# Optimization experiments

Measured on AMD Instinct MI355X. Metric: run time of the kernel, lower is better.

## Reference

```python
import jax, jax.numpy as jnp
import numpy as np

B = 32768
SF = 40  # subframe_size


def _gru_cell(x, h, wih, whh):
    # PyTorch GRUCell (bias=False): gates ordered [r; z; n]
    gi = x @ wih.T
    gh = h @ whh.T
    ir, iz, inn = jnp.split(gi, 3, axis=-1)
    hr, hz, hn = jnp.split(gh, 3, axis=-1)
    r = jax.nn.sigmoid(ir + hr)
    z = jax.nn.sigmoid(iz + hz)
    n = jnp.tanh(inn + r * hn)
    return (1.0 - z) * n + z * h


def setup_inputs() -> dict:
    key = jax.random.key(0)
    ks = iter(jax.random.split(key, 32))

    def rn(shape, scale=None):
        s = scale if scale is not None else 1.0 / np.sqrt(shape[-1])
        return (jax.random.normal(next(ks), shape, dtype=jnp.float32) * s)

    inp = {
        'cond': rn((B, 80), 1.0),
        'prev_pred': rn((B, 256), 1.0),
        'exc_mem': rn((B, 256), 1.0),
        'period': 32.0 + 223.0 * jax.random.uniform(next(ks), (B,), dtype=jnp.float32),
        's1': rn((B, 160), 1.0),
        's2': rn((B, 128), 1.0),
        's3': rn((B, 128), 1.0),
        's4': rn((B, 164), 1.0),
        'w_gain': rn((1, 80)),
        'b_gain': jnp.zeros((1,), jnp.float32),
        'w_fwc0': rn((192, 328)),
        'w_fwc0_glu': rn((192, 192)),
        'wih1': rn((480, 272)),
        'whh1': rn((480, 160)),
        'wglu1': rn((160, 160)),
        'wih2': rn((384, 240)),
        'whh2': rn((384, 128)),
        'wglu2': rn((128, 128)),
        'wih3': rn((384, 208)),
        'whh3': rn((384, 128)),
        'wglu3': rn((128, 128)),
        'w_skip': rn((128, 688)),
        'w_skip_glu': rn((128, 128)),
        'w_sig': rn((40, 128)),
        'w_pg': rn((4, 192)),
        'b_pg': jnp.zeros((4,), jnp.float32),
    }
    return inp


def reference(cond, prev_pred, exc_mem, period, s1, s2, s3, s4,
              w_gain, b_gain, w_fwc0, w_fwc0_glu,
              wih1, whh1, wglu1, wih2, whh2, wglu2, wih3, whh3, wglu3,
              w_skip, w_skip_glu, w_sig, w_pg, b_pg):
    # eval mode (training=False): quantization noise is identity; compat_mode=False path
    dt = cond.dtype
    period = jnp.clip(jnp.nan_to_num(period, nan=128.0, posinf=128.0, neginf=128.0), 32.0, 255.0)
    rng = jnp.arange(SF + 4, dtype=dt)
    # fractional pitch lookup with linear interpolation into exc_mem
    idxf = 256.0 - period[:, None] + rng[None, :] - 2.0  # [B, SF+4]
    idx0 = jnp.floor(idxf)
    alpha = jnp.clip(idxf - idx0, 0.0, 1.0)
    W = exc_mem.shape[1]
    i0 = jnp.mod(jnp.clip(idx0, 0.0, 255.0).astype(jnp.int32), W)
    i1 = jnp.mod(jnp.clip(idx0 + 1.0, 0.0, 255.0).astype(jnp.int32), W)
    v0 = jnp.take_along_axis(exc_mem, i0, axis=1)
    v1 = jnp.take_along_axis(exc_mem, i1, axis=1)
    pred = (1.0 - alpha) * v0 + alpha * v1  # [B, SF+4]

    # bounded gain
    gain = 0.2 + 0.8 * jax.nn.sigmoid(cond @ w_gain.T + b_gain)
    gain = jnp.clip(jnp.nan_to_num(gain, nan=1.0, posinf=20.0, neginf=1e-3), 1e-3, 20.0)
    inv = 1.0 / (1e-5 + gain)
    pred_n = pred * inv
    prev = exc_mem[:, -SF:] * inv
    tmp = jnp.concatenate([cond, pred_n, prev], axis=1)  # [B, 164]
    fpitch = pred_n[:, 2:-2]  # [B, SF]

    # FWConv: linear over cat(state, x), tanh, GLU
    xcat = jnp.concatenate([s4, tmp], axis=1)  # [B, 328]
    fw = jnp.tanh(xcat @ w_fwc0.T)
    fwc0_out = fw * jax.nn.sigmoid(fw @ w_fwc0_glu.T)  # [B, 192]
    new_s4 = tmp

    pitch_gain = jax.nn.sigmoid(fwc0_out @ w_pg.T + b_pg)  # [B, 4]

    h1 = _gru_cell(jnp.concatenate([fwc0_out, pitch_gain[:, 0:1] * fpitch, prev], 1), s1, wih1, whh1)
    g1 = h1 * jax.nn.sigmoid(h1 @ wglu1.T)
    h2 = _gru_cell(jnp.concatenate([g1, pitch_gain[:, 1:2] * fpitch, prev], 1), s2, wih2, whh2)
    g2 = h2 * jax.nn.sigmoid(h2 @ wglu2.T)
    h3 = _gru_cell(jnp.concatenate([g2, pitch_gain[:, 2:3] * fpitch, prev], 1), s3, wih3, whh3)
    g3 = h3 * jax.nn.sigmoid(h3 @ wglu3.T)

    skip_in = jnp.concatenate([g1, g2, g3, fwc0_out, pitch_gain[:, 3:4] * fpitch, prev], 1)  # [B, 688]
    sk = jnp.tanh(skip_in @ w_skip.T)
    sk = sk * jax.nn.sigmoid(sk @ w_skip_glu.T)
    sig_out = jnp.tanh(sk @ w_sig.T) * gain  # [B, SF]

    exc_mem_new = jnp.concatenate([exc_mem[:, SF:], sig_out], 1)
    prev_pred_new = jnp.concatenate([prev_pred[:, SF:], pred[:, 2:2 + SF]], 1)
    return sig_out, exc_mem_new, prev_pred_new, h1, h2, h3, new_s4
```

## Files before the change

kernel.cpp:

```cpp
#include <hip/hip_runtime.h>
#include <cstdint>
#include <cmath>

#define BTOT 32768L
#define OSIG 0L
#define OEXC (BTOT*40L)
#define OPREV (OEXC + BTOT*256L)
#define OH1 (OPREV + BTOT*256L)
#define OH2 (OH1 + BTOT*160L)
#define OH3 (OH2 + BTOT*128L)
#define ONS4 (OH3 + BTOT*128L)

typedef __attribute__((ext_vector_type(8))) short short8;
typedef __attribute__((ext_vector_type(4))) short short4v;
typedef __attribute__((ext_vector_type(4))) float f32x4;

#define AP 968


#define W_F0     0L
#define W_F0G    67584L
#define W_PG     104448L
#define W_IH1R   107520L
#define W_IH1Z   162816L
#define W_IH1N   218112L
#define W_HH1R   273408L
#define W_HH1Z   310272L
#define W_HH1N   347136L
#define W_GLU1   384000L
#define W_IH2R   420864L
#define W_IH2Z   453632L
#define W_IH2N   486400L
#define W_HH2R   519168L
#define W_HH2Z   535552L
#define W_HH2N   551936L
#define W_GLU2   568320L
#define W_IH3R   584704L
#define W_IH3Z   613376L
#define W_IH3N   642048L
#define W_HH3R   670720L
#define W_HH3Z   687104L
#define W_HH3N   703488L
#define W_GLU3   719872L
#define W_SKIP   736256L
#define W_SKIPG  859136L
#define W_SIG    875520L

__device__ __forceinline__ float sigm(float x){ return 1.0f/(1.0f+__expf(-x)); }
__device__ __forceinline__ float tanh_f(float x){
    float e = __expf(2.0f*x);
    return 1.0f - 2.0f/(e+1.0f);
}
__device__ __forceinline__ uint16_t f2bf(float x){
    union { float f; uint32_t u; } v; v.f = x;
    uint32_t r = v.u + 0x7FFFu + ((v.u>>16)&1u);
    return (uint16_t)(r>>16);
}
__device__ __forceinline__ float bf2f(uint16_t h){
    union { float f; uint32_t u; } v; v.u = ((uint32_t)h)<<16;
    return v.f;
}
__device__ __forceinline__ short4v pack4(float4 v){
    short4v r;
    r.x=(short)f2bf(v.x); r.y=(short)f2bf(v.y); r.z=(short)f2bf(v.z); r.w=(short)f2bf(v.w);
    return r;
}

struct PrepArgs { const float* s[15]; };

__global__ __launch_bounds__(64) void prep_kernel(PrepArgs pa, uint16_t* dst){
    static const long J[27][8] = {
        {0,  0,192,328,352,192, W_F0,   0},
        {1,  0,192,192,192,192, W_F0G,  0},
        {13, 0,  4,192,192, 16, W_PG,   0},
        {2,  0,160,272,288,192, W_IH1R, 0},
        {2,160,160,272,288,192, W_IH1Z, 0},
        {2,320,160,272,288,192, W_IH1N, 0},
        {3,  0,160,160,192,192, W_HH1R, 0},
        {3,160,160,160,192,192, W_HH1Z, 0},
        {3,320,160,160,192,192, W_HH1N, 0},
        {4,  0,160,160,192,192, W_GLU1, 0},
        {5,  0,128,240,256,128, W_IH2R, 0},
        {5,128,128,240,256,128, W_IH2Z, 0},
        {5,256,128,240,256,128, W_IH2N, 0},
        {6,  0,128,128,128,128, W_HH2R, 0},
        {6,128,128,128,128,128, W_HH2Z, 0},
        {6,256,128,128,128,128, W_HH2N, 0},
        {7,  0,128,128,128,128, W_GLU2, 0},
        {8,  0,128,208,224,128, W_IH3R, 0},
        {8,128,128,208,224,128, W_IH3Z, 0},
        {8,256,128,208,224,128, W_IH3N, 0},
        {9,  0,128,128,128,128, W_HH3R, 0},
        {9,128,128,128,128,128, W_HH3Z, 0},
        {9,256,128,128,128,128, W_HH3N, 0},
        {10, 0,128,128,128,128, W_GLU3, 0},
        {11, 0,128,688,960,128, W_SKIP, 1},
        {12, 0,128,128,128,128, W_SKIPG,0},
        {14, 0, 40,128,128, 64, W_SIG,  0},
    };
    long row = blockIdx.x;
    int j = 0;
    while (row >= J[j][5]) { row -= J[j][5]; ++j; }
    const float* src = pa.s[J[j][0]];
    const long ro = J[j][1], N = J[j][2], K = J[j][3], KP = J[j][4];
    const int type = (int)J[j][7];
    uint16_t* d = dst + J[j][6] + row*KP;
    for (long k = threadIdx.x; k < KP; k += 64){
        float v = 0.0f;
        if (row < N){
            if (type == 0){
                if (k < K) v = src[(ro+row)*K + k];
            } else {
                long s = -1;
                if (k < 192) s = 416 + k;
                else if (k >= 232 && k < 272) s = 648 + (k-232);
                else if (k >= 288 && k < 448) s = (k-288);
                else if (k >= 544 && k < 672) s = 160 + (k-544);
                else if (k >= 768 && k < 896) s = 288 + (k-768);
                else if (k >= 896 && k < 936) s = 608 + (k-896);
                if (s >= 0) v = src[row*688 + s];
            }
        }
        d[k] = f2bf(v);
    }
}

template<int KS, int CNT>
__device__ __forceinline__ void wgemm4(f32x4 (&acc)[CNT][4],
    const uint16_t* __restrict__ Bw, int KP,
    const uint16_t* A, int P, int w, int r16, int g)
{
    constexpr int T = KS*CNT;
    constexpr int PF = (T < 6) ? T : 6;
    const uint16_t* ap = A + r16*P + g*8;
    const uint16_t* bbase = Bw + (size_t)(w*16 + r16)*KP + g*8;
    short8 ring[PF];
    #pragma unroll
    for (int t=0;t<PF;++t)
        ring[t] = *(const short8*)(bbase + (size_t)(t%CNT)*128*KP + (size_t)(t/CNT)*32);
    short8 af[4];
    #pragma unroll
    for (int t=0;t<T;++t){
        const int s = t/CNT, i = t%CNT;
        if (i==0){
            #pragma unroll
            for (int mt=0;mt<4;++mt) af[mt] = *(const short8*)(ap + mt*16*P + s*32);
        }
        short8 bf = ring[t%PF];
        if (t+PF < T)
            ring[t%PF] = *(const short8*)(bbase + (size_t)((t+PF)%CNT)*128*KP + (size_t)((t+PF)/CNT)*32);
        #pragma unroll
        for (int mt=0;mt<4;++mt)
            acc[i][mt] = __builtin_amdgcn_mfma_f32_16x16x32_bf16(af[mt], bf, acc[i][mt],0,0,0);
    }
}
template<int CNT> __device__ __forceinline__ void zacc(f32x4 (&a)[CNT][4]){
    f32x4 z4 = {0.f,0.f,0.f,0.f};
    #pragma unroll
    for (int i=0;i<CNT;++i){
        #pragma unroll
        for (int mt=0;mt<4;++mt) a[i][mt]=z4;
    }
}

template<int CNT>
__device__ __forceinline__ void gru1_h(const uint16_t* __restrict__ W, uint16_t* ACTp,
    const float* __restrict__ s1g, float* __restrict__ out,
    float (&hk)[2][4][4], int row0, int w, int r16, int g)
{
    f32x4 gx[CNT][4], gh[CNT][4], ra[CNT][4], za[CNT][4];
    zacc(gx); zacc(gh); zacc(ra); zacc(za);
    wgemm4<9,CNT>(gx, W+W_IH1N, 288, ACTp,     AP, w,r16,g);
    wgemm4<9,CNT>(ra, W+W_IH1R, 288, ACTp,     AP, w,r16,g);
    wgemm4<9,CNT>(za, W+W_IH1Z, 288, ACTp,     AP, w,r16,g);
    wgemm4<6,CNT>(gh, W+W_HH1N, 192, ACTp+544, AP, w,r16,g);
    wgemm4<6,CNT>(ra, W+W_HH1R, 192, ACTp+544, AP, w,r16,g);
    wgemm4<6,CNT>(za, W+W_HH1Z, 192, ACTp+544, AP, w,r16,g);
    #pragma unroll
    for (int i=0;i<CNT;++i){
        int n = (w+8*i)*16 + r16;
        #pragma unroll
        for (int mt=0;mt<4;++mt){
            #pragma unroll
            for (int q=0;q<4;++q){
                int mrow = mt*16+g*4+q;
                float h = 0.f;
                if (n < 160){
                    float hpv = s1g[(long)(row0+mrow)*160 + n];
                    float r = sigm(ra[i][mt][q]);
                    float z = sigm(za[i][mt][q]);
                    float nn = tanh_f(gx[i][mt][q] + r*gh[i][mt][q]);
                    h = (1.f-z)*nn + z*hpv;
                    out[OH1 + (long)(row0+mrow)*160 + n] = h;
                }
                hk[i][mt][q] = h;
                ACTp[mrow*AP+768+n] = f2bf(h);
            }
        }
    }
}
template<int CNT>
__device__ __forceinline__ void glu1(const uint16_t* __restrict__ W, uint16_t* ACTp,
                                     float (&hk)[2][4][4], int w, int r16, int g){
    f32x4 gl[CNT][4];
    zacc(gl);
    wgemm4<6,CNT>(gl, W+W_GLU1, 192, ACTp+768, AP, w,r16,g);
    #pragma unroll
    for (int i=0;i<CNT;++i){
        int n = (w+8*i)*16 + r16;
        if (n < 160){
            #pragma unroll
            for (int mt=0;mt<4;++mt)
                #pragma unroll
                for (int q=0;q<4;++q){
                    int mrow = mt*16+g*4+q;
                    ACTp[mrow*AP + 288 + n] = f2bf(hk[i][mt][q]*sigm(gl[i][mt][q]));
                }
        }
    }
}

template<int KSX, int KSH>
__device__ __forceinline__ void gru23_h(
    const uint16_t* __restrict__ Wxr, const uint16_t* __restrict__ Wxz, const uint16_t* __restrict__ Wxn, int KPX,
    const uint16_t* __restrict__ Whr, const uint16_t* __restrict__ Whz, const uint16_t* __restrict__ Whn, int KPH,
    const uint16_t* XA, const uint16_t* HA, int HAP,
    const float* __restrict__ sg, float* __restrict__ outp, long obase,
    uint16_t* HBdst, int HBpitch,
    float (&hk)[4][4], int row0, int w, int r16, int g)
{
    const int n = w*16 + r16;
    f32x4 gx[1][4], gh[1][4], ra[1][4], za[1][4];
    zacc(gx); zacc(gh); zacc(ra); zacc(za);
    wgemm4<KSX,1>(gx, Wxn, KPX, XA, AP, w,r16,g);
    wgemm4<KSX,1>(ra, Wxr, KPX, XA, AP, w,r16,g);
    wgemm4<KSX,1>(za, Wxz, KPX, XA, AP, w,r16,g);
    wgemm4<KSH,1>(gh, Whn, KPH, HA, HAP, w,r16,g);
    wgemm4<KSH,1>(ra, Whr, KPH, HA, HAP, w,r16,g);
    wgemm4<KSH,1>(za, Whz, KPH, HA, HAP, w,r16,g);
    #pragma unroll
    for (int mt=0;mt<4;++mt){
        #pragma unroll
        for (int q=0;q<4;++q){
            int mrow = mt*16+g*4+q;
            float hpv = sg[(long)(row0+mrow)*128 + n];
            float r = sigm(ra[0][mt][q]), z = sigm(za[0][mt][q]);
            float nn = tanh_f(gx[0][mt][q] + r*gh[0][mt][q]);
            float h = (1.f-z)*nn + z*hpv;
            outp[obase + (long)(row0+mrow)*128 + n] = h;
            hk[mt][q] = h;
            if (HBdst) HBdst[mrow*HBpitch + n] = f2bf(h);
        }
    }
}

extern "C" __global__ __launch_bounds__(512, 2)
void fargan_mfma(const float* __restrict__ cond, const float* __restrict__ prev_pred,
                 const float* __restrict__ exc_mem, const float* __restrict__ period,
                 const float* __restrict__ s1, const float* __restrict__ s2,
                 const float* __restrict__ s3, const float* __restrict__ s4,
                 const float* __restrict__ w_gain, const float* __restrict__ b_gain,
                 const float* __restrict__ b_pg,
                 const uint16_t* __restrict__ W, float* __restrict__ out)
{
    __shared__ __align__(16) uint16_t ACT[64*AP];
    __shared__ __align__(16) uint16_t SH[64*136];
    __shared__ uint16_t FPITCHb[64*40];
    __shared__ float GAIN[64];
    __shared__ float PGs[64][4];

    const int tid = threadIdx.x;
    const int row0 = blockIdx.x * 64;
    const int w = tid >> 6, l = tid & 63, r16 = l & 15, g = l >> 4;
    const int rr = tid >> 3, c8 = tid & 7;
    const long grow = row0 + rr;

    const float* exc_row = exc_mem + grow*256;

    float a0 = 0.f;
    {
        const float4* c4 = (const float4*)(cond + grow*80);
        const float4* g4 = (const float4*)w_gain;
        float4* on4 = (float4*)(out + ONS4 + grow*164);
        for (int i=c8;i<20;i+=8){
            float4 cv = c4[i], gv = g4[i];
            a0 += cv.x*gv.x + cv.y*gv.y + cv.z*gv.z + cv.w*gv.w;
            *(short4v*)&ACT[rr*AP + 164 + 4*i] = pack4(cv);
            on4[i] = cv;
        }
    }
    a0 += __shfl_xor(a0,4,8); a0 += __shfl_xor(a0,2,8); a0 += __shfl_xor(a0,1,8);
    float gn = 0.2f + 0.8f*sigm(a0 + b_gain[0]);
    if (!(gn==gn)) gn = 1.0f;
    gn = fminf(fmaxf(gn, 0.001f), 20.0f);
    float inv = 1.0f/(1e-5f+gn);
    if (c8==0) GAIN[rr] = gn;

    float p = period[grow];
    p = (fabsf(p) <= 3.0e38f) ? p : 128.0f;
    p = fminf(fmaxf(p, 32.0f), 255.0f);

    for (int e=c8;e<44;e+=8){
        float idxf = 254.0f - p + (float)e;
        float idx0 = floorf(idxf);
        float al = fminf(fmaxf(idxf-idx0, 0.f), 1.f);
        int i0 = (int)fminf(fmaxf(idx0, 0.f), 255.f);
        int i1 = (int)fminf(fmaxf(idx0+1.f, 0.f), 255.f);
        float pr = (1.f-al)*exc_row[i0] + al*exc_row[i1];
        float pn = pr*inv;
        ACT[rr*AP + 244 + e] = f2bf(pn);
        out[ONS4 + grow*164 + 80 + e] = pn;
        if (e>=2 && e<42){
            out[OPREV + grow*256 + 216 + (e-2)] = pr;
            FPITCHb[rr*40 + (e-2)] = f2bf(pn);
        }
    }
    {
        const float4* pv4 = (const float4*)(exc_row + 216);
        float4* onp = (float4*)(out + ONS4 + grow*164 + 124);
        for (int i=c8;i<10;i+=8){
            float4 v = pv4[i];
            v.x*=inv; v.y*=inv; v.z*=inv; v.w*=inv;
            *(short4v*)&ACT[rr*AP + 288 + 4*i] = pack4(v);
            onp[i] = v;
        }
    }
    {
        const float4* s44 = (const float4*)(s4 + grow*164);
        for (int i=c8;i<41;i+=8)
            *(short4v*)&ACT[rr*AP + 4*i] = pack4(s44[i]);
        const float4* s14 = (const float4*)(s1 + grow*160);
        for (int i=c8;i<40;i+=8)
            *(short4v*)&ACT[rr*AP + 544 + 4*i] = pack4(s14[i]);
    }
    for (int i=328+c8;i<352;i+=8) ACT[rr*AP + i] = 0;
    for (int i=704+c8;i<736;i+=8) ACT[rr*AP + i] = 0;
    {
        const float4* pp4 = (const float4*)(prev_pred + grow*256 + 40);
        const float4* ex4 = (const float4*)(exc_row + 40);
        float4* op4 = (float4*)(out + OPREV + grow*256);
        float4* oe4 = (float4*)(out + OEXC + grow*256);
        for (int i=c8;i<54;i+=8){ op4[i] = pp4[i]; oe4[i] = ex4[i]; }
    }
    __syncthreads();

    float fwk[2][4][4];

    if (w < 4){
        f32x4 av[2][4]; zacc(av);
        wgemm4<11,2>(av, W+W_F0, 352, ACT, AP, w,r16,g);
        #pragma unroll
        for (int i=0;i<2;++i){
            int n = (w+8*i)*16 + r16;
            #pragma unroll
            for (int mt=0;mt<4;++mt)
                #pragma unroll
                for (int q=0;q<4;++q){
                    int mrow = mt*16+g*4+q;
                    float t = tanh_f(av[i][mt][q]);
                    fwk[i][mt][q] = t;
                    ACT[mrow*AP+352+n] = f2bf(t);
                }
        }
    } else {
        f32x4 av[1][4]; zacc(av);
        wgemm4<11,1>(av, W+W_F0, 352, ACT, AP, w,r16,g);
        int n = w*16 + r16;
        #pragma unroll
        for (int mt=0;mt<4;++mt)
            #pragma unroll
            for (int q=0;q<4;++q){
                int mrow = mt*16+g*4+q;
                float t = tanh_f(av[0][mt][q]);
                fwk[0][mt][q] = t;
                ACT[mrow*AP+352+n] = f2bf(t);
            }
    }
    __syncthreads();

    if (w < 4){
        f32x4 av[2][4]; zacc(av);
        wgemm4<6,2>(av, W+W_F0G, 192, ACT+352, AP, w,r16,g);
        #pragma unroll
        for (int i=0;i<2;++i){
            int n = (w+8*i)*16 + r16;
            #pragma unroll
            for (int mt=0;mt<4;++mt)
                #pragma unroll
                for (int q=0;q<4;++q){
                    int mrow = mt*16+g*4+q;
                    ACT[mrow*AP+n] = f2bf(fwk[i][mt][q]*sigm(av[i][mt][q]));
                }
        }
    } else {
        f32x4 av[1][4]; zacc(av);
        wgemm4<6,1>(av, W+W_F0G, 192, ACT+352, AP, w,r16,g);
        int n = w*16 + r16;
        #pragma unroll
        for (int mt=0;mt<4;++mt)
            #pragma unroll
            for (int q=0;q<4;++q){
                int mrow = mt*16+g*4+q;
                ACT[mrow*AP+n] = f2bf(fwk[0][mt][q]*sigm(av[0][mt][q]));
            }
    }
    __syncthreads();

    {
        f32x4 av[1][4]; zacc(av);
        wgemm4<6,1>(av, W+W_PG, 192, ACT, AP, 0, r16, g);
        if (w==0 && r16<4){
            float bp = b_pg[r16];
            #pragma unroll
            for (int mt=0;mt<4;++mt)
                #pragma unroll
                for (int q=0;q<4;++q)
                    PGs[mt*16+g*4+q][r16] = sigm(av[0][mt][q] + bp);
        }
    }
    __syncthreads();

    for (int i=c8;i<40;i+=8){
        ACT[rr*AP+192+i] = f2bf(PGs[rr][0]*bf2f(FPITCHb[rr*40+i]));
        ACT[rr*AP+232+i] = ACT[rr*AP+288+i];
    }
    __syncthreads();

    float hk1[2][4][4];
    if (w < 4) gru1_h<2>(W, ACT, s1, out, hk1, row0, w,r16,g);
    else       gru1_h<1>(W, ACT, s1, out, hk1, row0, w,r16,g);
    __syncthreads();

    if (w < 4) glu1<2>(W, ACT, hk1, w,r16,g); else glu1<1>(W, ACT, hk1, w,r16,g);
    {
        const float4* s24 = (const float4*)(s2 + grow*128);
        for (int i=c8;i<32;i+=8)
            *(short4v*)&ACT[rr*AP + 544 + 4*i] = pack4(s24[i]);
    }
    for (int i=c8;i<40;i+=8){
        ACT[rr*AP+448+i] = f2bf(PGs[rr][1]*bf2f(FPITCHb[rr*40+i]));
        ACT[rr*AP+488+i] = ACT[rr*AP+232+i];
    }
    for (int i=528+c8;i<544;i+=8) ACT[rr*AP+i] = 0;
    __syncthreads();

    float hk[4][4];
    gru23_h<8,4>(W+W_IH2R, W+W_IH2Z, W+W_IH2N, 256,
                 W+W_HH2R, W+W_HH2Z, W+W_HH2N, 128,
                 ACT+288, ACT+544, AP, s2, out, OH2,
                 ACT+768, AP, hk, row0, w,r16,g);
    __syncthreads();

    {
        f32x4 gl[1][4]; zacc(gl);
        wgemm4<4,1>(gl, W+W_GLU2, 128, ACT+768, AP, w,r16,g);
        int n = w*16 + r16;
        #pragma unroll
        for (int mt=0;mt<4;++mt)
            #pragma unroll
            for (int q=0;q<4;++q){
                int mrow = mt*16+g*4+q;
                ACT[mrow*AP+544+n] = f2bf(hk[mt][q]*sigm(gl[0][mt][q]));
            }
    }
    {
        const float4* s34 = (const float4*)(s3 + grow*128);
        for (int i=c8;i<32;i+=8)
            *(short4v*)&SH[rr*136 + 4*i] = pack4(s34[i]);
    }
    for (int i=c8;i<40;i+=8){
        ACT[rr*AP+672+i] = f2bf(PGs[rr][2]*bf2f(FPITCHb[rr*40+i]));
        ACT[rr*AP+712+i] = ACT[rr*AP+232+i];
    }
    for (int i=752+c8;i<768;i+=8) ACT[rr*AP+i] = 0;
    __syncthreads();

    gru23_h<7,4>(W+W_IH3R, W+W_IH3Z, W+W_IH3N, 224,
                 W+W_HH3R, W+W_HH3Z, W+W_HH3N, 128,
                 ACT+544, SH, 136, s3, out, OH3,
                 (uint16_t*)nullptr, 0, hk, row0, w,r16,g);
    __syncthreads();

    {
        int n = w*16 + r16;
        #pragma unroll
        for (int mt=0;mt<4;++mt)
            #pragma unroll
            for (int q=0;q<4;++q)
                SH[(mt*16+g*4+q)*136 + n] = f2bf(hk[mt][q]);
    }
    __syncthreads();

    {
        f32x4 gl[1][4]; zacc(gl);
        {
            const uint16_t* ap = SH + r16*136 + g*8;
            const uint16_t* bbase = W + W_GLU3 + (size_t)(w*16 + r16)*128 + g*8;
            short8 ring[4];
            #pragma unroll
            for (int t=0;t<4;++t) ring[t] = *(const short8*)(bbase + t*32);
            #pragma unroll
            for (int s=0;s<4;++s){
                short8 af[4];
                #pragma unroll
                for (int mt=0;mt<4;++mt) af[mt] = *(const short8*)(ap + mt*16*136 + s*32);
                short8 bf = ring[s];
                #pragma unroll
                for (int mt=0;mt<4;++mt)
                    gl[0][mt] = __builtin_amdgcn_mfma_f32_16x16x32_bf16(af[mt], bf, gl[0][mt],0,0,0);
            }
        }
        int n = w*16 + r16;
        #pragma unroll
        for (int mt=0;mt<4;++mt)
            #pragma unroll
            for (int q=0;q<4;++q){
                int mrow = mt*16+g*4+q;
                ACT[mrow*AP+768+n] = f2bf(hk[mt][q]*sigm(gl[0][mt][q]));
            }
    }
    for (int i=c8;i<40;i+=8)
        ACT[rr*AP+896+i] = f2bf(PGs[rr][3]*bf2f(FPITCHb[rr*40+i]));
    __syncthreads();

    float skk[4][4];
    {
        f32x4 av[1][4]; zacc(av);
        wgemm4<30,1>(av, W+W_SKIP, 960, ACT, AP, w,r16,g);
        int n = w*16 + r16;
        #pragma unroll
        for (int mt=0;mt<4;++mt)
            #pragma unroll
            for (int q=0;q<4;++q){
                int mrow = mt*16+g*4+q;
                float t = tanh_f(av[0][mt][q]);
                skk[mt][q] = t;
                SH[mrow*136+n] = f2bf(t);
            }
    }
    __syncthreads();
    {
        f32x4 av[1][4]; zacc(av);
        {
            const uint16_t* ap = SH + r16*136 + g*8;
            const uint16_t* bbase = W + W_SKIPG + (size_t)(w*16 + r16)*128 + g*8;
            short8 ring[4];
            #pragma unroll
            for (int t=0;t<4;++t) ring[t] = *(const short8*)(bbase + t*32);
            #pragma unroll
            for (int s=0;s<4;++s){
                short8 af[4];
                #pragma unroll
                for (int mt=0;mt<4;++mt) af[mt] = *(const short8*)(ap + mt*16*136 + s*32);
                short8 bf = ring[s];
                #pragma unroll
                for (int mt=0;mt<4;++mt)
                    av[0][mt] = __builtin_amdgcn_mfma_f32_16x16x32_bf16(af[mt], bf, av[0][mt],0,0,0);
            }
        }
        int n = w*16 + r16;
        #pragma unroll
        for (int mt=0;mt<4;++mt)
            #pragma unroll
            for (int q=0;q<4;++q){
                int mrow = mt*16+g*4+q;
                ACT[mrow*AP+n] = f2bf(skk[mt][q]*sigm(av[0][mt][q]));
            }
    }
    __syncthreads();
    if (w < 4){
        f32x4 av[1][4]; zacc(av);
        wgemm4<4,1>(av, W+W_SIG, 128, ACT, AP, w,r16,g);
        int n = w*16 + r16;
        if (n < 40){
            #pragma unroll
            for (int mt=0;mt<4;++mt)
                #pragma unroll
                for (int q=0;q<4;++q){
                    int mrow = mt*16+g*4+q;
                    float sv = tanh_f(av[0][mt][q]) * GAIN[mrow];
                    out[OSIG + (long)(row0+mrow)*40 + n] = sv;
                    out[OEXC + (long)(row0+mrow)*256 + 216 + n] = sv;
                }
        }
    }
}

extern "C" void kernel_launch(void* const* d_in, const int* in_sizes, int n_in,
                              void* d_out, int out_size, void* d_ws, size_t ws_size,
                              hipStream_t stream) {
    const float* cond      = (const float*)d_in[0];
    const float* prev_pred = (const float*)d_in[1];
    const float* exc_mem   = (const float*)d_in[2];
    const float* period    = (const float*)d_in[3];
    const float* s1        = (const float*)d_in[4];
    const float* s2        = (const float*)d_in[5];
    const float* s3        = (const float*)d_in[6];
    const float* s4        = (const float*)d_in[7];
    const float* w_gain    = (const float*)d_in[8];
    const float* b_gain    = (const float*)d_in[9];
    const float* w_fwc0    = (const float*)d_in[10];
    const float* w_fwc0_glu= (const float*)d_in[11];
    const float* wih1      = (const float*)d_in[12];
    const float* whh1      = (const float*)d_in[13];
    const float* wglu1     = (const float*)d_in[14];
    const float* wih2      = (const float*)d_in[15];
    const float* whh2      = (const float*)d_in[16];
    const float* wglu2     = (const float*)d_in[17];
    const float* wih3      = (const float*)d_in[18];
    const float* whh3      = (const float*)d_in[19];
    const float* wglu3     = (const float*)d_in[20];
    const float* w_skip    = (const float*)d_in[21];
    const float* w_skip_glu= (const float*)d_in[22];
    const float* w_sig     = (const float*)d_in[23];
    const float* w_pg      = (const float*)d_in[24];
    const float* b_pg      = (const float*)d_in[25];
    float* out = (float*)d_out;
    uint16_t* wsbf = (uint16_t*)d_ws;

    PrepArgs pa;
    pa.s[0]=w_fwc0; pa.s[1]=w_fwc0_glu; pa.s[2]=wih1; pa.s[3]=whh1; pa.s[4]=wglu1;
    pa.s[5]=wih2; pa.s[6]=whh2; pa.s[7]=wglu2; pa.s[8]=wih3; pa.s[9]=whh3;
    pa.s[10]=wglu3; pa.s[11]=w_skip; pa.s[12]=w_skip_glu; pa.s[13]=w_pg; pa.s[14]=w_sig;

    hipLaunchKernelGGL(prep_kernel, dim3(3856), dim3(64), 0, stream, pa, wsbf);
    hipLaunchKernelGGL(fargan_mfma, dim3(512), dim3(512), 0, stream,
        cond, prev_pred, exc_mem, period, s1, s2, s3, s4,
        w_gain, b_gain, b_pg, wsbf, out);
}
```

Baseline: 227.7 us.

## Halve per-block batch rows to 32 and double grid for occupancy

Shrinks each workgroup's batch tile from 64 to 32 rows, halving the MFMA accumulator tiles per wave and shared-memory footprint, doubles the grid to 1024 blocks, and raises launch bounds to allow 4 blocks per CU. Thread-to-row mapping for the elementwise staging loops changes from 8 to 16 threads per row. It also swaps the manual bf16 rounding for the HIP intrinsic. Each weight fragment now feeds half as many MFMAs, so weight load traffic per row doubles; the goal is more parallelism across the 256 CUs and better latency hiding.

```diff
diff --git a/kernel.cpp b/kernel.cpp
--- a/kernel.cpp
+++ b/kernel.cpp
@@ -1,4 +1,5 @@
 #include <hip/hip_runtime.h>
+#include <hip/hip_bf16.h>
 #include <cstdint>
 #include <cmath>
 
@@ -16,7 +17,6 @@
 typedef __attribute__((ext_vector_type(4))) float f32x4;
 
 #define AP 968
-
 
 #define W_F0     0L
 #define W_F0G    67584L
@@ -52,9 +52,8 @@
     return 1.0f - 2.0f/(e+1.0f);
 }
 __device__ __forceinline__ uint16_t f2bf(float x){
-    union { float f; uint32_t u; } v; v.f = x;
-    uint32_t r = v.u + 0x7FFFu + ((v.u>>16)&1u);
-    return (uint16_t)(r>>16);
+    __hip_bfloat16 h = __float2bfloat16(x);
+    return *(uint16_t*)&h;
 }
 __device__ __forceinline__ float bf2f(uint16_t h){
     union { float f; uint32_t u; } v; v.u = ((uint32_t)h)<<16;
@@ -126,7 +125,7 @@
 }
 
 template<int KS, int CNT>
-__device__ __forceinline__ void wgemm4(f32x4 (&acc)[CNT][4],
+__device__ __forceinline__ void wgemm4(f32x4 (&acc)[CNT][2],
     const uint16_t* __restrict__ Bw, int KP,
     const uint16_t* A, int P, int w, int r16, int g)
 {
@@ -138,37 +137,37 @@
     #pragma unroll
     for (int t=0;t<PF;++t)
         ring[t] = *(const short8*)(bbase + (size_t)(t%CNT)*128*KP + (size_t)(t/CNT)*32);
-    short8 af[4];
+    short8 af[2];
     #pragma unroll
     for (int t=0;t<T;++t){
         const int s = t/CNT, i = t%CNT;
         if (i==0){
             #pragma unroll
-            for (int mt=0;mt<4;++mt) af[mt] = *(const short8*)(ap + mt*16*P + s*32);
+            for (int mt=0;mt<2;++mt) af[mt] = *(const short8*)(ap + mt*16*P + s*32);
         }
         short8 bf = ring[t%PF];
         if (t+PF < T)
             ring[t%PF] = *(const short8*)(bbase + (size_t)((t+PF)%CNT)*128*KP + (size_t)((t+PF)/CNT)*32);
         #pragma unroll
-        for (int mt=0;mt<4;++mt)
+        for (int mt=0;mt<2;++mt)
             acc[i][mt] = __builtin_amdgcn_mfma_f32_16x16x32_bf16(af[mt], bf, acc[i][mt],0,0,0);
     }
 }
-template<int CNT> __device__ __forceinline__ void zacc(f32x4 (&a)[CNT][4]){
+template<int CNT> __device__ __forceinline__ void zacc(f32x4 (&a)[CNT][2]){
     f32x4 z4 = {0.f,0.f,0.f,0.f};
     #pragma unroll
     for (int i=0;i<CNT;++i){
         #pragma unroll
-        for (int mt=0;mt<4;++mt) a[i][mt]=z4;
+        for (int mt=0;mt<2;++mt) a[i][mt]=z4;
     }
 }
 
 template<int CNT>
 __device__ __forceinline__ void gru1_h(const uint16_t* __restrict__ W, uint16_t* ACTp,
     const float* __restrict__ s1g, float* __restrict__ out,
-    float (&hk)[2][4][4], int row0, int w, int r16, int g)
+    float (&hk)[2][2][4], int row0, int w, int r16, int g)
 {
-    f32x4 gx[CNT][4], gh[CNT][4], ra[CNT][4], za[CNT][4];
+    f32x4 gx[CNT][2], gh[CNT][2], ra[CNT][2], za[CNT][2];
     zacc(gx); zacc(gh); zacc(ra); zacc(za);
     wgemm4<9,CNT>(gx, W+W_IH1N, 288, ACTp,     AP, w,r16,g);
     wgemm4<9,CNT>(ra, W+W_IH1R, 288, ACTp,     AP, w,r16,g);
@@ -180,7 +179,7 @@
     for (int i=0;i<CNT;++i){
         int n = (w+8*i)*16 + r16;
         #pragma unroll
-        for (int mt=0;mt<4;++mt){
+        for (int mt=0;mt<2;++mt){
             #pragma unroll
             for (int q=0;q<4;++q){
                 int mrow = mt*16+g*4+q;
@@ -201,8 +200,8 @@
 }
 template<int CNT>
 __device__ __forceinline__ void glu1(const uint16_t* __restrict__ W, uint16_t* ACTp,
-                                     float (&hk)[2][4][4], int w, int r16, int g){
-    f32x4 gl[CNT][4];
+                                     float (&hk)[2][2][4], int w, int r16, int g){
+    f32x4 gl[CNT][2];
     zacc(gl);
     wgemm4<6,CNT>(gl, W+W_GLU1, 192, ACTp+768, AP, w,r16,g);
     #pragma unroll
@@ -210,7 +209,7 @@
         int n = (w+8*i)*16 + r16;
         if (n < 160){
             #pragma unroll
-            for (int mt=0;mt<4;++mt)
+            for (int mt=0;mt<2;++mt)
                 #pragma unroll
                 for (int q=0;q<4;++q){
                     int mrow = mt*16+g*4+q;
@@ -227,10 +226,10 @@
     const uint16_t* XA, const uint16_t* HA, int HAP,
     const float* __restrict__ sg, float* __restrict__ outp, long obase,
     uint16_t* HBdst, int HBpitch,
-    float (&hk)[4][4], int row0, int w, int r16, int g)
+    float (&hk)[2][4], int row0, int w, int r16, int g)
 {
     const int n = w*16 + r16;
-    f32x4 gx[1][4], gh[1][4], ra[1][4], za[1][4];
+    f32x4 gx[1][2], gh[1][2], ra[1][2], za[1][2];
     zacc(gx); zacc(gh); zacc(ra); zacc(za);
     wgemm4<KSX,1>(gx, Wxn, KPX, XA, AP, w,r16,g);
     wgemm4<KSX,1>(ra, Wxr, KPX, XA, AP, w,r16,g);
@@ -239,7 +238,7 @@
     wgemm4<KSH,1>(ra, Whr, KPH, HA, HAP, w,r16,g);
     wgemm4<KSH,1>(za, Whz, KPH, HA, HAP, w,r16,g);
     #pragma unroll
-    for (int mt=0;mt<4;++mt){
+    for (int mt=0;mt<2;++mt){
         #pragma unroll
         for (int q=0;q<4;++q){
             int mrow = mt*16+g*4+q;
@@ -254,7 +253,7 @@
     }
 }
 
-extern "C" __global__ __launch_bounds__(512, 2)
+extern "C" __global__ __launch_bounds__(512, 4)
 void fargan_mfma(const float* __restrict__ cond, const float* __restrict__ prev_pred,
                  const float* __restrict__ exc_mem, const float* __restrict__ period,
                  const float* __restrict__ s1, const float* __restrict__ s2,
@@ -263,16 +262,16 @@
                  const float* __restrict__ b_pg,
                  const uint16_t* __restrict__ W, float* __restrict__ out)
 {
-    __shared__ __align__(16) uint16_t ACT[64*AP];
-    __shared__ __align__(16) uint16_t SH[64*136];
-    __shared__ uint16_t FPITCHb[64*40];
-    __shared__ float GAIN[64];
-    __shared__ float PGs[64][4];
+    __shared__ __align__(16) uint16_t ACT[32*AP];
+    __shared__ __align__(16) uint16_t SH[32*136];
+    __shared__ uint16_t FPITCHb[32*40];
+    __shared__ float GAIN[32];
+    __shared__ float PGs[32][4];
 
     const int tid = threadIdx.x;
-    const int row0 = blockIdx.x * 64;
+    const int row0 = blockIdx.x * 32;
     const int w = tid >> 6, l = tid & 63, r16 = l & 15, g = l >> 4;
-    const int rr = tid >> 3, c8 = tid & 7;
+    const int rr = tid >> 4, c16 = tid & 15;
     const long grow = row0 + rr;
 
     const float* exc_row = exc_mem + grow*256;
@@ -282,25 +281,26 @@
         const float4* c4 = (const float4*)(cond + grow*80);
         const float4* g4 = (const float4*)w_gain;
         float4* on4 = (float4*)(out + ONS4 + grow*164);
-        for (int i=c8;i<20;i+=8){
+        for (int i=c16;i<20;i+=16){
             float4 cv = c4[i], gv = g4[i];
             a0 += cv.x*gv.x + cv.y*gv.y + cv.z*gv.z + cv.w*gv.w;
             *(short4v*)&ACT[rr*AP + 164 + 4*i] = pack4(cv);
             on4[i] = cv;
         }
     }
-    a0 += __shfl_xor(a0,4,8); a0 += __shfl_xor(a0,2,8); a0 += __shfl_xor(a0,1,8);
+    a0 += __shfl_xor(a0,8,16); a0 += __shfl_xor(a0,4,16);
+    a0 += __shfl_xor(a0,2,16); a0 += __shfl_xor(a0,1,16);
     float gn = 0.2f + 0.8f*sigm(a0 + b_gain[0]);
     if (!(gn==gn)) gn = 1.0f;
     gn = fminf(fmaxf(gn, 0.001f), 20.0f);
     float inv = 1.0f/(1e-5f+gn);
-    if (c8==0) GAIN[rr] = gn;
+    if (c16==0) GAIN[rr] = gn;
 
     float p = period[grow];
     p = (fabsf(p) <= 3.0e38f) ? p : 128.0f;
     p = fminf(fmaxf(p, 32.0f), 255.0f);
 
-    for (int e=c8;e<44;e+=8){
+    for (int e=c16;e<44;e+=16){
         float idxf = 254.0f - p + (float)e;
         float idx0 = floorf(idxf);
         float al = fminf(fmaxf(idxf-idx0, 0.f), 1.f);
@@ -318,7 +318,7 @@
     {
         const float4* pv4 = (const float4*)(exc_row + 216);
         float4* onp = (float4*)(out + ONS4 + grow*164 + 124);
-        for (int i=c8;i<10;i+=8){
+        for (int i=c16;i<10;i+=16){
             float4 v = pv4[i];
             v.x*=inv; v.y*=inv; v.z*=inv; v.w*=inv;
             *(short4v*)&ACT[rr*AP + 288 + 4*i] = pack4(v);
@@ -327,33 +327,33 @@
     }
     {
         const float4* s44 = (const float4*)(s4 + grow*164);
-        for (int i=c8;i<41;i+=8)
+        for (int i=c16;i<41;i+=16)
             *(short4v*)&ACT[rr*AP + 4*i] = pack4(s44[i]);
         const float4* s14 = (const float4*)(s1 + grow*160);
-        for (int i=c8;i<40;i+=8)
+        for (int i=c16;i<40;i+=16)
             *(short4v*)&ACT[rr*AP + 544 + 4*i] = pack4(s14[i]);
     }
-    for (int i=328+c8;i<352;i+=8) ACT[rr*AP + i] = 0;
-    for (int i=704+c8;i<736;i+=8) ACT[rr*AP + i] = 0;
+    for (int i=328+c16;i<352;i+=16) ACT[rr*AP + i] = 0;
+    for (int i=704+c16;i<736;i+=16) ACT[rr*AP + i] = 0;
     {
         const float4* pp4 = (const float4*)(prev_pred + grow*256 + 40);
         const float4* ex4 = (const float4*)(exc_row + 40);
         float4* op4 = (float4*)(out + OPREV + grow*256);
         float4* oe4 = (float4*)(out + OEXC + grow*256);
-        for (int i=c8;i<54;i+=8){ op4[i] = pp4[i]; oe4[i] = ex4[i]; }
-    }
-    __syncthreads();
-
-    float fwk[2][4][4];
+        for (int i=c16;i<54;i+=16){ op4[i] = pp4[i]; oe4[i] = ex4[i]; }
+    }
+    __syncthreads();
+
+    float fwk[2][2][4];
 
     if (w < 4){
-        f32x4 av[2][4]; zacc(av);
+        f32x4 av[2][2]; zacc(av);
         wgemm4<11,2>(av, W+W_F0, 352, ACT, AP, w,r16,g);
         #pragma unroll
         for (int i=0;i<2;++i){
             int n = (w+8*i)*16 + r16;
             #pragma unroll
-            for (int mt=0;mt<4;++mt)
+            for (int mt=0;mt<2;++mt)
                 #pragma unroll
                 for (int q=0;q<4;++q){
                     int mrow = mt*16+g*4+q;
@@ -363,11 +363,11 @@
                 }
         }
     } else {
-        f32x4 av[1][4]; zacc(av);
+        f32x4 av[1][2]; zacc(av);
         wgemm4<11,1>(av, W+W_F0, 352, ACT, AP, w,r16,g);
         int n = w*16 + r16;
         #pragma unroll
-        for (int mt=0;mt<4;++mt)
+        for (int mt=0;mt<2;++mt)
             #pragma unroll
             for (int q=0;q<4;++q){
                 int mrow = mt*16+g*4+q;
@@ -379,13 +379,13 @@
     __syncthreads();
 
     if (w < 4){
-        f32x4 av[2][4]; zacc(av);
+        f32x4 av[2][2]; zacc(av);
         wgemm4<6,2>(av, W+W_F0G, 192, ACT+352, AP, w,r16,g);
         #pragma unroll
         for (int i=0;i<2;++i){
             int n = (w+8*i)*16 + r16;
             #pragma unroll
-            for (int mt=0;mt<4;++mt)
+            for (int mt=0;mt<2;++mt)
                 #pragma unroll
                 for (int q=0;q<4;++q){
                     int mrow = mt*16+g*4+q;
@@ -393,11 +393,11 @@
                 }
         }
     } else {
-        f32x4 av[1][4]; zacc(av);
+        f32x4 av[1][2]; zacc(av);
         wgemm4<6,1>(av, W+W_F0G, 192, ACT+352, AP, w,r16,g);
         int n = w*16 + r16;
         #pragma unroll
-        for (int mt=0;mt<4;++mt)
+        for (int mt=0;mt<2;++mt)
             #pragma unroll
             for (int q=0;q<4;++q){
                 int mrow = mt*16+g*4+q;
@@ -407,12 +407,12 @@
     __syncthreads();
 
     {
-        f32x4 av[1][4]; zacc(av);
+        f32x4 av[1][2]; zacc(av);
         wgemm4<6,1>(av, W+W_PG, 192, ACT, AP, 0, r16, g);
         if (w==0 && r16<4){
             float bp = b_pg[r16];
             #pragma unroll
-            for (int mt=0;mt<4;++mt)
+            for (int mt=0;mt<2;++mt)
                 #pragma unroll
                 for (int q=0;q<4;++q)
                     PGs[mt*16+g*4+q][r16] = sigm(av[0][mt][q] + bp);
@@ -420,13 +420,13 @@
     }
     __syncthreads();
 
-    for (int i=c8;i<40;i+=8){
+    for (int i=c16;i<40;i+=16){
         ACT[rr*AP+192+i] = f2bf(PGs[rr][0]*bf2f(FPITCHb[rr*40+i]));
         ACT[rr*AP+232+i] = ACT[rr*AP+288+i];
     }
     __syncthreads();
 
-    float hk1[2][4][4];
+    float hk1[2][2][4];
     if (w < 4) gru1_h<2>(W, ACT, s1, out, hk1, row0, w,r16,g);
     else       gru1_h<1>(W, ACT, s1, out, hk1, row0, w,r16,g);
     __syncthreads();
@@ -434,17 +434,17 @@
     if (w < 4) glu1<2>(W, ACT, hk1, w,r16,g); else glu1<1>(W, ACT, hk1, w,r16,g);
     {
         const float4* s24 = (const float4*)(s2 + grow*128);
-        for (int i=c8;i<32;i+=8)
+        for (int i=c16;i<32;i+=16)
             *(short4v*)&ACT[rr*AP + 544 + 4*i] = pack4(s24[i]);
     }
-    for (int i=c8;i<40;i+=8){
+    for (int i=c16;i<40;i+=16){
         ACT[rr*AP+448+i] = f2bf(PGs[rr][1]*bf2f(FPITCHb[rr*40+i]));
         ACT[rr*AP+488+i] = ACT[rr*AP+232+i];
     }
-    for (int i=528+c8;i<544;i+=8) ACT[rr*AP+i] = 0;
-    __syncthreads();
-
-    float hk[4][4];
+    for (int i=528+c16;i<544;i+=16) ACT[rr*AP+i] = 0;
+    __syncthreads();
+
+    float hk[2][4];
     gru23_h<8,4>(W+W_IH2R, W+W_IH2Z, W+W_IH2N, 256,
                  W+W_HH2R, W+W_HH2Z, W+W_HH2N, 128,
                  ACT+288, ACT+544, AP, s2, out, OH2,
@@ -452,11 +452,11 @@
     __syncthreads();
 
     {
-        f32x4 gl[1][4]; zacc(gl);
+        f32x4 gl[1][2]; zacc(gl);
         wgemm4<4,1>(gl, W+W_GLU2, 128, ACT+768, AP, w,r16,g);
         int n = w*16 + r16;
         #pragma unroll
-        for (int mt=0;mt<4;++mt)
+        for (int mt=0;mt<2;++mt)
             #pragma unroll
             for (int q=0;q<4;++q){
                 int mrow = mt*16+g*4+q;
@@ -465,14 +465,14 @@
     }
     {
         const float4* s34 = (const float4*)(s3 + grow*128);
-        for (int i=c8;i<32;i+=8)
+        for (int i=c16;i<32;i+=16)
             *(short4v*)&SH[rr*136 + 4*i] = pack4(s34[i]);
     }
-    for (int i=c8;i<40;i+=8){
+    for (int i=c16;i<40;i+=16){
         ACT[rr*AP+672+i] = f2bf(PGs[rr][2]*bf2f(FPITCHb[rr*40+i]));
         ACT[rr*AP+712+i] = ACT[rr*AP+232+i];
     }
-    for (int i=752+c8;i<768;i+=8) ACT[rr*AP+i] = 0;
+    for (int i=752+c16;i<768;i+=16) ACT[rr*AP+i] = 0;
     __syncthreads();
 
     gru23_h<7,4>(W+W_IH3R, W+W_IH3Z, W+W_IH3N, 224,
@@ -484,7 +484,7 @@
     {
         int n = w*16 + r16;
         #pragma unroll
-        for (int mt=0;mt<4;++mt)
+        for (int mt=0;mt<2;++mt)
             #pragma unroll
             for (int q=0;q<4;++q)
                 SH[(mt*16+g*4+q)*136 + n] = f2bf(hk[mt][q]);
@@ -492,7 +492,7 @@
     __syncthreads();
 
     {
-        f32x4 gl[1][4]; zacc(gl);
+        f32x4 gl[1][2]; zacc(gl);
         {
             const uint16_t* ap = SH + r16*136 + g*8;
             const uint16_t* bbase = W + W_GLU3 + (size_t)(w*16 + r16)*128 + g*8;
@@ -501,35 +501,35 @@
             for (int t=0;t<4;++t) ring[t] = *(const short8*)(bbase + t*32);
             #pragma unroll
             for (int s=0;s<4;++s){
-                short8 af[4];
-                #pragma unroll
-                for (int mt=0;mt<4;++mt) af[mt] = *(const short8*)(ap + mt*16*136 + s*32);
+                short8 af[2];
+                #pragma unroll
+                for (int mt=0;mt<2;++mt) af[mt] = *(const short8*)(ap + mt*16*136 + s*32);
                 short8 bf = ring[s];
                 #pragma unroll
-                for (int mt=0;mt<4;++mt)
+                for (int mt=0;mt<2;++mt)
                     gl[0][mt] = __builtin_amdgcn_mfma_f32_16x16x32_bf16(af[mt], bf, gl[0][mt],0,0,0);
             }
         }
         int n = w*16 + r16;
         #pragma unroll
-        for (int mt=0;mt<4;++mt)
+        for (int mt=0;mt<2;++mt)
             #pragma unroll
             for (int q=0;q<4;++q){
                 int mrow = mt*16+g*4+q;
                 ACT[mrow*AP+768+n] = f2bf(hk[mt][q]*sigm(gl[0][mt][q]));
             }
     }
-    for (int i=c8;i<40;i+=8)
+    for (int i=c16;i<40;i+=16)
         ACT[rr*AP+896+i] = f2bf(PGs[rr][3]*bf2f(FPITCHb[rr*40+i]));
     __syncthreads();
 
-    float skk[4][4];
-    {
-        f32x4 av[1][4]; zacc(av);
+    float skk[2][4];
+    {
+        f32x4 av[1][2]; zacc(av);
         wgemm4<30,1>(av, W+W_SKIP, 960, ACT, AP, w,r16,g);
         int n = w*16 + r16;
         #pragma unroll
-        for (int mt=0;mt<4;++mt)
+        for (int mt=0;mt<2;++mt)
             #pragma unroll
             for (int q=0;q<4;++q){
                 int mrow = mt*16+g*4+q;
@@ -540,7 +540,7 @@
     }
     __syncthreads();
     {
-        f32x4 av[1][4]; zacc(av);
+        f32x4 av[1][2]; zacc(av);
         {
             const uint16_t* ap = SH + r16*136 + g*8;
             const uint16_t* bbase = W + W_SKIPG + (size_t)(w*16 + r16)*128 + g*8;
@@ -549,18 +549,18 @@
             for (int t=0;t<4;++t) ring[t] = *(const short8*)(bbase + t*32);
             #pragma unroll
             for (int s=0;s<4;++s){
-                short8 af[4];
-                #pragma unroll
-                for (int mt=0;mt<4;++mt) af[mt] = *(const short8*)(ap + mt*16*136 + s*32);
+                short8 af[2];
+                #pragma unroll
+                for (int mt=0;mt<2;++mt) af[mt] = *(const short8*)(ap + mt*16*136 + s*32);
                 short8 bf = ring[s];
                 #pragma unroll
-                for (int mt=0;mt<4;++mt)
+                for (int mt=0;mt<2;++mt)
                     av[0][mt] = __builtin_amdgcn_mfma_f32_16x16x32_bf16(af[mt], bf, av[0][mt],0,0,0);
             }
         }
         int n = w*16 + r16;
         #pragma unroll
-        for (int mt=0;mt<4;++mt)
+        for (int mt=0;mt<2;++mt)
             #pragma unroll
             for (int q=0;q<4;++q){
                 int mrow = mt*16+g*4+q;
@@ -569,12 +569,12 @@
     }
     __syncthreads();
     if (w < 4){
-        f32x4 av[1][4]; zacc(av);
+        f32x4 av[1][2]; zacc(av);
         wgemm4<4,1>(av, W+W_SIG, 128, ACT, AP, w,r16,g);
         int n = w*16 + r16;
         if (n < 40){
             #pragma unroll
-            for (int mt=0;mt<4;++mt)
+            for (int mt=0;mt<2;++mt)
                 #pragma unroll
                 for (int q=0;q<4;++q){
                     int mrow = mt*16+g*4+q;
@@ -624,7 +624,7 @@
     pa.s[10]=wglu3; pa.s[11]=w_skip; pa.s[12]=w_skip_glu; pa.s[13]=w_pg; pa.s[14]=w_sig;
 
     hipLaunchKernelGGL(prep_kernel, dim3(3856), dim3(64), 0, stream, pa, wsbf);
-    hipLaunchKernelGGL(fargan_mfma, dim3(512), dim3(512), 0, stream,
+    hipLaunchKernelGGL(fargan_mfma, dim3(1024), dim3(512), 0, stream,
         cond, prev_pred, exc_mem, period, s1, s2, s3, s4,
         w_gain, b_gain, b_pg, wsbf, out);
 }
```

Measured after the change: 272.1 us. 19.5% more time.
